# Optimization experiments

Hardware: AMD Instinct MI355X
Metric: run time of the kernel (lower is better)

## Reference

```python
import jax, jax.numpy as jnp
import numpy as np

D_MODEL = 2048
NUM_HEADS = 16
D_K = D_MODEL // NUM_HEADS
LORA_R = 8
LORA_ALPHA = 16
SCALING = LORA_ALPHA / LORA_R  # 2.0
B, S = 2, 2048


def setup_inputs() -> dict:
    key = jax.random.key(0)
    ks = jax.random.split(key, 17)
    s = 1.0 / np.sqrt(D_MODEL)
    d = {"x": jax.random.normal(ks[0], (B, S, D_MODEL), jnp.float32)}
    i = 1
    for name in ("q", "k", "v", "o"):
        d[f"W{name}"] = jax.random.uniform(ks[i], (D_MODEL, D_MODEL), jnp.float32, -s, s); i += 1
        d[f"b{name}"] = jax.random.uniform(ks[i], (D_MODEL,), jnp.float32, -s, s); i += 1
        d[f"A{name}"] = jax.random.uniform(ks[i], (LORA_R, D_MODEL), jnp.float32, -s, s); i += 1
        # lora_B is zero-initialized in the module, but use small random so grads flow meaningfully
        d[f"B{name}"] = jax.random.normal(ks[i], (D_MODEL, LORA_R), jnp.float32) * 0.01; i += 1
    return d


def _lora_linear(x, W, b, A, Bm):
    # F.linear(x, W, b) + (x @ A.T @ B.T) * scaling
    return x @ W.T + b + ((x @ A.T) @ Bm.T) * SCALING


def reference(x, Wq, bq, Aq, Bq, Wk, bk, Ak, Bk, Wv, bv, Av, Bv, Wo, bo, Ao, Bo):
    batch = x.shape[0]
    q = _lora_linear(x, Wq, bq, Aq, Bq)
    k = _lora_linear(x, Wk, bk, Ak, Bk)
    v = _lora_linear(x, Wv, bv, Av, Bv)
    # [B, S, H, Dk] -> [B, H, S, Dk]
    q = q.reshape(batch, -1, NUM_HEADS, D_K).transpose(0, 2, 1, 3)
    k = k.reshape(batch, -1, NUM_HEADS, D_K).transpose(0, 2, 1, 3)
    v = v.reshape(batch, -1, NUM_HEADS, D_K).transpose(0, 2, 1, 3)
    scores = jnp.einsum("bhqd,bhkd->bhqk", q, k) / jnp.sqrt(jnp.float32(D_K))
    attn = jax.nn.softmax(scores, axis=-1)
    context = jnp.einsum("bhqk,bhkd->bhqd", attn, v)
    context = context.transpose(0, 2, 1, 3).reshape(batch, -1, D_MODEL)
    return _lora_linear(context, Wo, bo, Ao, Bo)
```

## Files before the change

### kernel.cpp

```cpp
#include <hip/hip_runtime.h>
#include <stdint.h>

typedef unsigned short u16;
typedef unsigned int   u32;
typedef __bf16  bf16x8 __attribute__((ext_vector_type(8)));
typedef float   f32x4  __attribute__((ext_vector_type(4)));

#define LORA_SCALE 2.0f
#define QSCALE 0.08838834764831845f
#define LOG2E  1.4426950408889634f
#define RESCALE_THR 8.0f

__device__ __forceinline__ u16 f2bf(float f){
  u32 u = __builtin_bit_cast(u32, f);
  u32 r = (u + 0x7fffu + ((u >> 16) & 1u)) >> 16;
  return (u16)r;
}
__device__ __forceinline__ float bf2f(u16 v){
  return __builtin_bit_cast(float, ((u32)v) << 16);
}
__device__ __forceinline__ u32 cvt_pk_bf16(float lo, float hi){
  u32 d;
  asm("v_cvt_pk_bf16_f32 %0, %1, %2" : "=v"(d) : "v"(lo), "v"(hi));
  return d;
}

typedef __attribute__((address_space(3))) u32 lds_u32_t;
typedef __attribute__((address_space(1))) const u32 g_u32_t;

__device__ __forceinline__ void gload16(const void* g, void* l){
  __builtin_amdgcn_global_load_lds((g_u32_t*)(unsigned long long)g,
                                   (lds_u32_t*)(u32)(unsigned long long)l,
                                   16, 0, 0);
}

__global__ __launch_bounds__(256) void cvt_f32_bf16(const float* __restrict__ in,
                                                    u16* __restrict__ out, int n){
  int i = (blockIdx.x * 256 + threadIdx.x) * 8;
  if (i >= n) return;
  float4 a = *(const float4*)(in + i);
  float4 b = *(const float4*)(in + i + 4);
  u16 o[8] = {f2bf(a.x),f2bf(a.y),f2bf(a.z),f2bf(a.w),
              f2bf(b.x),f2bf(b.y),f2bf(b.z),f2bf(b.w)};
  *(uint4*)(out + i) = *(const uint4*)o;
}

template<int NG, int BF16IN>
__global__ __launch_bounds__(256) void lora_xa_kernel(const void* __restrict__ xin,
    const float* __restrict__ A0, const float* __restrict__ A1, const float* __restrict__ A2,
    float* __restrict__ xout){
  int w = threadIdx.x >> 6, lane = threadIdx.x & 63;
  int m = blockIdx.x * 4 + w;
  float acc[NG][8];
  #pragma unroll
  for (int g=0; g<NG; ++g)
    #pragma unroll
    for (int r=0; r<8; ++r) acc[g][r] = 0.f;
  const float* As[3] = {A0, A1, A2};
  #pragma unroll 1
  for (int it=0; it<8; ++it){
    int k = it*256 + lane*4;
    float4 xv;
    if (BF16IN){
      const u16* xp = (const u16*)xin + (size_t)m*2048 + k;
      ushort4 u = *(const ushort4*)xp;
      xv.x = bf2f(u.x); xv.y = bf2f(u.y); xv.z = bf2f(u.z); xv.w = bf2f(u.w);
    } else {
      xv = *(const float4*)((const float*)xin + (size_t)m*2048 + k);
    }
    #pragma unroll
    for (int g=0; g<NG; ++g){
      const float* Ag = As[g];
      #pragma unroll
      for (int r=0; r<8; ++r){
        float4 av = *(const float4*)(Ag + r*2048 + k);
        acc[g][r] += xv.x*av.x + xv.y*av.y + xv.z*av.z + xv.w*av.w;
      }
    }
  }
  #pragma unroll
  for (int g=0; g<NG; ++g)
    #pragma unroll
    for (int r=0; r<8; ++r){
      float v = acc[g][r];
      #pragma unroll
      for (int off=32; off; off>>=1) v += __shfl_xor(v, off);
      if (lane == 0) xout[g*32768 + m*8 + r] = v;
    }
}

__global__ __launch_bounds__(256, 2) void gemm_fused(
    const u16* __restrict__ A, const u16* __restrict__ W,
    const float* __restrict__ bias, const float* __restrict__ lB,
    const float* __restrict__ xa, void* __restrict__ outp,
    int f32out, int swz, float oscale){
  const int Kd = 2048, Nd = 2048;
  __shared__ u16 Ash[128*32];
  __shared__ u16 Bsh[128*32];
  int tid = threadIdx.x, w = tid >> 6, lane = tid & 63;
  int l15 = lane & 15, l4 = lane >> 4;
  int n0 = blockIdx.x * 128, m0 = blockIdx.y * 128;
  int wm = w >> 1, wn = w & 1;
  f32x4 acc[4][4];
  #pragma unroll
  for (int mi=0; mi<4; mi++)
    #pragma unroll
    for (int ni=0; ni<4; ni++) acc[mi][ni] = (f32x4){0.f,0.f,0.f,0.f};

  const u16* Arow = A + (size_t)m0 * Kd;
  const u16* Wrow = W + (size_t)n0 * Kd;
  for (int kt = 0; kt < Kd; kt += 32){
    __syncthreads();
    #pragma unroll
    for (int i=0; i<2; ++i){
      int e = (i*256 + tid) * 8;
      int r = e >> 5, c = e & 31;
      gload16(Arow + (size_t)r*Kd + kt + c, (char*)Ash + i*4096 + w*1024);
      gload16(Wrow + (size_t)r*Kd + kt + c, (char*)Bsh + i*4096 + w*1024);
    }
    __syncthreads();
    bf16x8 af[4], bfv[4];
    #pragma unroll
    for (int mi=0; mi<4; mi++)
      af[mi] = *(const bf16x8*)(Ash + (wm*64 + mi*16 + l15)*32 + l4*8);
    #pragma unroll
    for (int ni=0; ni<4; ni++)
      bfv[ni] = *(const bf16x8*)(Bsh + (wn*64 + ni*16 + l15)*32 + l4*8);
    #pragma unroll
    for (int mi=0; mi<4; mi++)
      #pragma unroll
      for (int ni=0; ni<4; ni++)
        acc[mi][ni] = __builtin_amdgcn_mfma_f32_16x16x32_bf16(af[mi], bfv[ni], acc[mi][ni], 0, 0, 0);
  }
  float bv[4]; float4 lb0[4], lb1[4];
  #pragma unroll
  for (int ni=0; ni<4; ni++){
    int col = n0 + wn*64 + ni*16 + l15;
    bv[ni] = bias[col];
    lb0[ni] = *(const float4*)(lB + col*8);
    lb1[ni] = *(const float4*)(lB + col*8 + 4);
  }
  #pragma unroll
  for (int mi=0; mi<4; mi++)
    #pragma unroll
    for (int j=0; j<4; j++){
      int r = m0 + wm*64 + mi*16 + l4*4 + j;
      float4 xv0 = *(const float4*)(xa + (size_t)r*8);
      float4 xv1 = *(const float4*)(xa + (size_t)r*8 + 4);
      #pragma unroll
      for (int ni=0; ni<4; ni++){
        int col = n0 + wn*64 + ni*16 + l15;
        float v = acc[mi][ni][j] + bv[ni] + LORA_SCALE * (
            xv0.x*lb0[ni].x + xv0.y*lb0[ni].y + xv0.z*lb0[ni].z + xv0.w*lb0[ni].w +
            xv1.x*lb1[ni].x + xv1.y*lb1[ni].y + xv1.z*lb1[ni].z + xv1.w*lb1[ni].w);
        v *= oscale;
        if (f32out){
          ((float*)outp)[(size_t)r*Nd + col] = v;
        } else {
          int cs = swz ? (col ^ ((r & 7) << 3)) : col;
          ((u16*)outp)[(size_t)r*Nd + cs] = f2bf(v);
        }
      }
    }
}

__global__ __launch_bounds__(256) void transpose_v(const u16* __restrict__ V,
                                                   u16* __restrict__ Vt){
  __shared__ u16 tile[64*80];
  int tid = threadIdx.x;
  int f0 = blockIdx.x * 64, m0 = blockIdx.y * 64;
  int i = tid >> 2, j0 = (tid & 3) * 16;
  #pragma unroll
  for (int kk=0; kk<16; kk+=8){
    uint4 u = *(const uint4*)(V + (size_t)(m0 + i)*2048 + f0 + j0 + kk);
    *(uint4*)(tile + i*80 + j0 + kk) = u;
  }
  __syncthreads();
  int j = tid >> 2, i0 = (tid & 3) * 16;
  int b = m0 >> 11, s0 = m0 & 2047;
  int h = f0 >> 7, d = (f0 & 127) + j;
  int c = (d & 7) << 3;
  size_t obase = ((size_t)((b*16 + h)*128 + d)) * 2048 + s0;
  #pragma unroll
  for (int kk=0; kk<16; kk+=8){
    u16 v8[8];
    #pragma unroll
    for (int u2=0; u2<8; ++u2) v8[u2] = tile[(i0+kk+u2)*80 + j];
    *(uint4*)(Vt + obase + ((i0+kk) ^ c)) = *(const uint4*)v8;
  }
}

__global__ __launch_bounds__(256, 2) void attn_kernel(
    const u16* __restrict__ Q, const u16* __restrict__ K,
    const u16* __restrict__ Vt, u16* __restrict__ ctx){
  __shared__ u16 buf[2][16384];
  __shared__ u16 Psh[4*32*64];
  int tid = threadIdx.x, w = tid >> 6, lane = tid & 63;
  int l15 = lane & 15, l4 = lane >> 4;
  int qt = blockIdx.x, bh = blockIdx.y;
  int b = bh >> 4, h = bh & 15;
  const u16* Qg = Q + (size_t)(b*2048 + qt*128) * 2048 + h*128;
  const u16* Kg = K + (size_t)(b*2048) * 2048 + h*128;
  const u16* Vg = Vt + (size_t)bh * 128 * 2048;

  #pragma unroll
  for (int i=0; i<8; ++i){
    int e = (i*256 + tid) * 8;
    int r = e >> 7, cc = e & 127;
    gload16(Qg + (size_t)r*2048 + cc, (char*)buf[1] + i*4096 + w*1024);
  }
  #pragma unroll
  for (int i=0; i<4; ++i){
    int e = (i*256 + tid) * 8;
    int r = e >> 7, cc = e & 127;
    gload16(Kg + (size_t)r*2048 + cc, (char*)buf[0] + i*4096 + w*1024);
    int dd = e >> 6, c2 = e & 63;
    gload16(Vg + (size_t)dd*2048 + c2, (char*)buf[0] + 16384 + i*4096 + w*1024);
  }
  __syncthreads();

  bf16x8 qf[2][4];
  #pragma unroll
  for (int mi=0; mi<2; mi++){
    int r = w*32 + mi*16 + l15;
    #pragma unroll
    for (int kb=0; kb<4; kb++){
      int cc = (kb*32 + l4*8) ^ ((r & 7) << 3);
      qf[mi][kb] = *(const bf16x8*)(buf[1] + r*128 + cc);
    }
  }
  __syncthreads();

  f32x4 ctxa[2][8];
  #pragma unroll
  for (int mi=0; mi<2; mi++)
    #pragma unroll
    for (int nd=0; nd<8; nd++) ctxa[mi][nd] = (f32x4){0.f,0.f,0.f,0.f};
  float mrun[2] = {-3.0e38f, -3.0e38f};
  float lrun[2] = {0.f, 0.f};

  char* PwB = (char*)(Psh + w * (32*64));
  int psw = (l15 & 7) << 4;

  for (int t = 0; t < 32; ++t){
    int cur = t & 1;
    const u16* Kc = buf[cur];
    const u16* Vc = buf[cur] + 8192;
    if (t + 1 < 32){
      int kvn = (t + 1) * 64;
      char* bn = (char*)buf[cur ^ 1];
      #pragma unroll
      for (int i=0; i<4; ++i){
        int e = (i*256 + tid) * 8;
        int r = e >> 7, cc = e & 127;
        gload16(Kg + (size_t)(kvn + r)*2048 + cc, bn + i*4096 + w*1024);
        int dd = e >> 6, c2 = e & 63;
        gload16(Vg + (size_t)dd*2048 + kvn + c2, bn + 16384 + i*4096 + w*1024);
      }
    }
    f32x4 s[2][4];
    #pragma unroll
    for (int mi=0; mi<2; mi++)
      #pragma unroll
      for (int ni=0; ni<4; ni++) s[mi][ni] = (f32x4){0.f,0.f,0.f,0.f};
    __builtin_amdgcn_s_setprio(1);
    #pragma unroll
    for (int kb=0; kb<4; kb++){
      #pragma unroll
      for (int ni=0; ni<4; ni++){
        int r = ni*16 + l15;
        int cc = (kb*32 + l4*8) ^ ((r & 7) << 3);
        bf16x8 kf = *(const bf16x8*)(Kc + r*128 + cc);
        s[0][ni] = __builtin_amdgcn_mfma_f32_16x16x32_bf16(kf, qf[0][kb], s[0][ni], 0, 0, 0);
        s[1][ni] = __builtin_amdgcn_mfma_f32_16x16x32_bf16(kf, qf[1][kb], s[1][ni], 0, 0, 0);
      }
    }
    __builtin_amdgcn_s_setprio(0);
    float pm[2];
    #pragma unroll
    for (int mi=0; mi<2; mi++){
      float v = s[mi][0][0];
      #pragma unroll
      for (int ni=0; ni<4; ni++)
        #pragma unroll
        for (int j=0; j<4; j++) v = fmaxf(v, s[mi][ni][j]);
      v = fmaxf(v, __shfl_xor(v, 16));
      v = fmaxf(v, __shfl_xor(v, 32));
      pm[mi] = v;
    }
    bool need = (pm[0] > mrun[0] + RESCALE_THR) || (pm[1] > mrun[1] + RESCALE_THR);
    if (__any(need)){
      #pragma unroll
      for (int mi=0; mi<2; mi++){
        float mnew = fmaxf(mrun[mi], pm[mi]);
        float cr = exp2f(mrun[mi] - mnew);
        lrun[mi] *= cr;
        mrun[mi] = mnew;
        #pragma unroll
        for (int nd=0; nd<8; nd++) ctxa[mi][nd] *= cr;
      }
    }
    #pragma unroll
    for (int mi=0; mi<2; mi++){
      float ps = 0.f;
      #pragma unroll
      for (int ni=0; ni<4; ni++){
        float p0 = exp2f(s[mi][ni][0] - mrun[mi]);
        float p1 = exp2f(s[mi][ni][1] - mrun[mi]);
        float p2 = exp2f(s[mi][ni][2] - mrun[mi]);
        float p3 = exp2f(s[mi][ni][3] - mrun[mi]);
        ps += (p0 + p1) + (p2 + p3);
        uint2 pk = {cvt_pk_bf16(p0, p1), cvt_pk_bf16(p2, p3)};
        *(uint2*)(PwB + (mi*16 + l15)*128 + ((ni*32 + l4*8) ^ psw)) = pk;
      }
      ps += __shfl_xor(ps, 16);
      ps += __shfl_xor(ps, 32);
      lrun[mi] += ps;
    }
    bf16x8 pb[2][2];
    #pragma unroll
    for (int mi=0; mi<2; mi++)
      #pragma unroll
      for (int kvb=0; kvb<2; kvb++)
        pb[mi][kvb] = *(const bf16x8*)(PwB + (mi*16 + l15)*128 + ((kvb*64 + l4*16) ^ psw));
    __builtin_amdgcn_s_setprio(1);
    #pragma unroll
    for (int nd=0; nd<8; nd++){
      int dd = nd*16 + l15;
      int sw = (dd & 7) << 3;
      #pragma unroll
      for (int kvb=0; kvb<2; kvb++){
        bf16x8 vf = *(const bf16x8*)(Vc + dd*64 + ((kvb*32 + l4*8) ^ sw));
        ctxa[0][nd] = __builtin_amdgcn_mfma_f32_16x16x32_bf16(vf, pb[0][kvb], ctxa[0][nd], 0, 0, 0);
        ctxa[1][nd] = __builtin_amdgcn_mfma_f32_16x16x32_bf16(vf, pb[1][kvb], ctxa[1][nd], 0, 0, 0);
      }
    }
    __builtin_amdgcn_s_setprio(0);
    __syncthreads();
  }
  char* OwB = (char*)buf[0] + w*8192;
  #pragma unroll
  for (int mi=0; mi<2; mi++){
    float inv = 1.0f / lrun[mi];
    #pragma unroll
    for (int nd=0; nd<8; nd++){
      f32x4 c = ctxa[mi][nd] * inv;
      uint2 pk = {cvt_pk_bf16(c[0], c[1]), cvt_pk_bf16(c[2], c[3])};
      *(uint2*)(OwB + (mi*16 + l15)*256 + ((nd*32 + l4*8) ^ psw)) = pk;
    }
  }
  #pragma unroll
  for (int i=0; i<8; ++i){
    int row = i*4 + l4;
    int colb = l15*16;
    uint4 v = *(const uint4*)(OwB + row*256 + (colb ^ ((row & 7) << 4)));
    int srow = qt*128 + w*32 + row;
    *(uint4*)(ctx + ((size_t)(b*2048 + srow))*2048 + h*128 + colb/2) = v;
  }
}

extern "C" void kernel_launch(void* const* d_in, const int* in_sizes, int n_in,
                              void* d_out, int out_size, void* d_ws, size_t ws_size,
                              hipStream_t stream){
  const float* x  = (const float*)d_in[0];
  const float* Wq = (const float*)d_in[1];  const float* bq = (const float*)d_in[2];
  const float* Aq = (const float*)d_in[3];  const float* Bq = (const float*)d_in[4];
  const float* Wk = (const float*)d_in[5];  const float* bk = (const float*)d_in[6];
  const float* Ak = (const float*)d_in[7];  const float* Bk = (const float*)d_in[8];
  const float* Wv = (const float*)d_in[9];  const float* bv = (const float*)d_in[10];
  const float* Av = (const float*)d_in[11]; const float* Bv = (const float*)d_in[12];
  const float* Wo = (const float*)d_in[13]; const float* bo = (const float*)d_in[14];
  const float* Ao = (const float*)d_in[15]; const float* Bo = (const float*)d_in[16];

  char* ws = (char*)d_ws;
  size_t off = 0;
  u16* xbf = (u16*)(ws + off); off += (size_t)4096*2048*2;
  u16* wqb = (u16*)(ws + off); off += (size_t)2048*2048*2;
  u16* wkb = (u16*)(ws + off); off += (size_t)2048*2048*2;
  u16* wvb = (u16*)(ws + off); off += (size_t)2048*2048*2;
  u16* wob = (u16*)(ws + off); off += (size_t)2048*2048*2;
  float* xa = (float*)(ws + off); off += (size_t)4*32768*4;
  u16* Qb  = (u16*)(ws + off); off += (size_t)4096*2048*2;
  u16* Kb  = (u16*)(ws + off); off += (size_t)4096*2048*2;
  u16* Vb  = (u16*)(ws + off); off += (size_t)4096*2048*2;
  u16* Vtb = (u16*)(ws + off); off += (size_t)4096*2048*2;
  if (ws_size < off) return;

  cvt_f32_bf16<<<4096, 256, 0, stream>>>(x,  xbf, 4096*2048);
  cvt_f32_bf16<<<2048, 256, 0, stream>>>(Wq, wqb, 2048*2048);
  cvt_f32_bf16<<<2048, 256, 0, stream>>>(Wk, wkb, 2048*2048);
  cvt_f32_bf16<<<2048, 256, 0, stream>>>(Wv, wvb, 2048*2048);
  cvt_f32_bf16<<<2048, 256, 0, stream>>>(Wo, wob, 2048*2048);

  lora_xa_kernel<3, 0><<<1024, 256, 0, stream>>>((const void*)x, Aq, Ak, Av, xa);

  gemm_fused<<<dim3(16,32), 256, 0, stream>>>(xbf, wqb, bq, Bq, xa,        Qb, 0, 1, QSCALE*LOG2E);
  gemm_fused<<<dim3(16,32), 256, 0, stream>>>(xbf, wkb, bk, Bk, xa+32768,  Kb, 0, 1, 1.0f);
  gemm_fused<<<dim3(16,32), 256, 0, stream>>>(xbf, wvb, bv, Bv, xa+65536,  Vb, 0, 0, 1.0f);

  transpose_v<<<dim3(32,64), 256, 0, stream>>>(Vb, Vtb);

  attn_kernel<<<dim3(16,32), 256, 0, stream>>>(Qb, Kb, Vtb, Vb);

  lora_xa_kernel<1, 1><<<1024, 256, 0, stream>>>((const void*)Vb, Ao, Ao, Ao, xa+98304);

  gemm_fused<<<dim3(16,32), 256, 0, stream>>>(Vb, wob, bo, Bo, xa+98304, d_out, 1, 0, 1.0f);
}
```

Before: 391.7 us.

## Fuse QKV projections into one GEMM launch and merge conversion kernels

The four weight conversions are merged into one launch, and the x-to-bf16 conversion is folded into the LoRA x@A kernel so x is read once. The Q, K and V GEMMs become a single 48x32-block launch over a concatenated bf16 weight buffer, with per-block selection of bias, LoRA B, scale and swizzle. The attention grid is remapped so consecutive blocks spread across heads, which is meant to improve L2 locality or load balance. Together these cut launch overhead and redundant x traffic and give the QKV GEMM more blocks in flight. The cost is extra per-block branching in the fused kernels.

```diff
diff --git a/kernel.cpp b/kernel.cpp
--- a/kernel.cpp
+++ b/kernel.cpp
@@ -34,42 +34,40 @@
                                    16, 0, 0);
 }
 
-__global__ __launch_bounds__(256) void cvt_f32_bf16(const float* __restrict__ in,
-                                                    u16* __restrict__ out, int n){
-  int i = (blockIdx.x * 256 + threadIdx.x) * 8;
-  if (i >= n) return;
-  float4 a = *(const float4*)(in + i);
-  float4 b = *(const float4*)(in + i + 4);
+__global__ __launch_bounds__(256) void cvt_w4(const float* __restrict__ W0,
+    const float* __restrict__ W1, const float* __restrict__ W2,
+    const float* __restrict__ W3, u16* __restrict__ wqkv, u16* __restrict__ wo){
+  int sel = blockIdx.x >> 11;
+  int inner = blockIdx.x & 2047;
+  const float* src = sel==0 ? W0 : sel==1 ? W1 : sel==2 ? W2 : W3;
+  u16* dst = sel<3 ? (wqkv + (size_t)sel*4194304) : wo;
+  int i = (inner*256 + threadIdx.x) * 8;
+  float4 a = *(const float4*)(src + i);
+  float4 b = *(const float4*)(src + i + 4);
   u16 o[8] = {f2bf(a.x),f2bf(a.y),f2bf(a.z),f2bf(a.w),
               f2bf(b.x),f2bf(b.y),f2bf(b.z),f2bf(b.w)};
-  *(uint4*)(out + i) = *(const uint4*)o;
-}
-
-template<int NG, int BF16IN>
-__global__ __launch_bounds__(256) void lora_xa_kernel(const void* __restrict__ xin,
+  *(uint4*)(dst + i) = *(const uint4*)o;
+}
+
+__global__ __launch_bounds__(256) void lora_x_fused(const float* __restrict__ x,
     const float* __restrict__ A0, const float* __restrict__ A1, const float* __restrict__ A2,
-    float* __restrict__ xout){
+    float* __restrict__ xout, u16* __restrict__ xbf){
   int w = threadIdx.x >> 6, lane = threadIdx.x & 63;
   int m = blockIdx.x * 4 + w;
-  float acc[NG][8];
-  #pragma unroll
-  for (int g=0; g<NG; ++g)
+  float acc[3][8];
+  #pragma unroll
+  for (int g=0; g<3; ++g)
     #pragma unroll
     for (int r=0; r<8; ++r) acc[g][r] = 0.f;
   const float* As[3] = {A0, A1, A2};
   #pragma unroll 1
   for (int it=0; it<8; ++it){
     int k = it*256 + lane*4;
-    float4 xv;
-    if (BF16IN){
-      const u16* xp = (const u16*)xin + (size_t)m*2048 + k;
-      ushort4 u = *(const ushort4*)xp;
-      xv.x = bf2f(u.x); xv.y = bf2f(u.y); xv.z = bf2f(u.z); xv.w = bf2f(u.w);
-    } else {
-      xv = *(const float4*)((const float*)xin + (size_t)m*2048 + k);
-    }
-    #pragma unroll
-    for (int g=0; g<NG; ++g){
+    float4 xv = *(const float4*)(x + (size_t)m*2048 + k);
+    u16 o[4] = {f2bf(xv.x), f2bf(xv.y), f2bf(xv.z), f2bf(xv.w)};
+    *(uint2*)(xbf + (size_t)m*2048 + k) = *(const uint2*)o;
+    #pragma unroll
+    for (int g=0; g<3; ++g){
       const float* Ag = As[g];
       #pragma unroll
       for (int r=0; r<8; ++r){
@@ -79,7 +77,7 @@
     }
   }
   #pragma unroll
-  for (int g=0; g<NG; ++g)
+  for (int g=0; g<3; ++g)
     #pragma unroll
     for (int r=0; r<8; ++r){
       float v = acc[g][r];
@@ -89,11 +87,116 @@
     }
 }
 
-__global__ __launch_bounds__(256, 2) void gemm_fused(
+__global__ __launch_bounds__(256) void lora_xa_bf16(const u16* __restrict__ xin,
+    const float* __restrict__ A0, float* __restrict__ xout){
+  int w = threadIdx.x >> 6, lane = threadIdx.x & 63;
+  int m = blockIdx.x * 4 + w;
+  float acc[8];
+  #pragma unroll
+  for (int r=0; r<8; ++r) acc[r] = 0.f;
+  #pragma unroll 1
+  for (int it=0; it<8; ++it){
+    int k = it*256 + lane*4;
+    ushort4 u = *(const ushort4*)(xin + (size_t)m*2048 + k);
+    float4 xv = {bf2f(u.x), bf2f(u.y), bf2f(u.z), bf2f(u.w)};
+    #pragma unroll
+    for (int r=0; r<8; ++r){
+      float4 av = *(const float4*)(A0 + r*2048 + k);
+      acc[r] += xv.x*av.x + xv.y*av.y + xv.z*av.z + xv.w*av.w;
+    }
+  }
+  #pragma unroll
+  for (int r=0; r<8; ++r){
+    float v = acc[r];
+    #pragma unroll
+    for (int off=32; off; off>>=1) v += __shfl_xor(v, off);
+    if (lane == 0) xout[m*8 + r] = v;
+  }
+}
+
+__global__ __launch_bounds__(256, 2) void gemm_qkv(
+    const u16* __restrict__ A, const u16* __restrict__ W,
+    const float* __restrict__ bq, const float* __restrict__ bk, const float* __restrict__ bv,
+    const float* __restrict__ lBq, const float* __restrict__ lBk, const float* __restrict__ lBv,
+    const float* __restrict__ xa, u16* __restrict__ Qb, u16* __restrict__ Kb, u16* __restrict__ Vb){
+  const int Kd = 2048;
+  __shared__ u16 Ash[128*32];
+  __shared__ u16 Bsh[128*32];
+  int tid = threadIdx.x, w = tid >> 6, lane = tid & 63;
+  int l15 = lane & 15, l4 = lane >> 4;
+  int n0g = blockIdx.x * 128, m0 = blockIdx.y * 128;
+  int which = blockIdx.x >> 4;
+  int n0 = n0g & 2047;
+  const float* bias = which==0 ? bq : which==1 ? bk : bv;
+  const float* lB   = which==0 ? lBq : which==1 ? lBk : lBv;
+  const float* xs   = xa + which*32768;
+  u16* outp         = which==0 ? Qb : which==1 ? Kb : Vb;
+  int swz = (which <= 1);
+  float oscale = (which == 0) ? QSCALE*LOG2E : 1.0f;
+  int wm = w >> 1, wn = w & 1;
+  f32x4 acc[4][4];
+  #pragma unroll
+  for (int mi=0; mi<4; mi++)
+    #pragma unroll
+    for (int ni=0; ni<4; ni++) acc[mi][ni] = (f32x4){0.f,0.f,0.f,0.f};
+
+  const u16* Arow = A + (size_t)m0 * Kd;
+  const u16* Wrow = W + (size_t)n0g * Kd;
+  for (int kt = 0; kt < Kd; kt += 32){
+    __syncthreads();
+    #pragma unroll
+    for (int i=0; i<2; ++i){
+      int e = (i*256 + tid) * 8;
+      int r = e >> 5, c = e & 31;
+      gload16(Arow + (size_t)r*Kd + kt + c, (char*)Ash + i*4096 + w*1024);
+      gload16(Wrow + (size_t)r*Kd + kt + c, (char*)Bsh + i*4096 + w*1024);
+    }
+    __syncthreads();
+    bf16x8 af[4], bfv[4];
+    #pragma unroll
+    for (int mi=0; mi<4; mi++)
+      af[mi] = *(const bf16x8*)(Ash + (wm*64 + mi*16 + l15)*32 + l4*8);
+    #pragma unroll
+    for (int ni=0; ni<4; ni++)
+      bfv[ni] = *(const bf16x8*)(Bsh + (wn*64 + ni*16 + l15)*32 + l4*8);
+    #pragma unroll
+    for (int mi=0; mi<4; mi++)
+      #pragma unroll
+      for (int ni=0; ni<4; ni++)
+        acc[mi][ni] = __builtin_amdgcn_mfma_f32_16x16x32_bf16(af[mi], bfv[ni], acc[mi][ni], 0, 0, 0);
+  }
+  float bvv[4]; float4 lb0[4], lb1[4];
+  #pragma unroll
+  for (int ni=0; ni<4; ni++){
+    int col = n0 + wn*64 + ni*16 + l15;
+    bvv[ni] = bias[col];
+    lb0[ni] = *(const float4*)(lB + col*8);
+    lb1[ni] = *(const float4*)(lB + col*8 + 4);
+  }
+  #pragma unroll
+  for (int mi=0; mi<4; mi++)
+    #pragma unroll
+    for (int j=0; j<4; j++){
+      int r = m0 + wm*64 + mi*16 + l4*4 + j;
+      float4 xv0 = *(const float4*)(xs + (size_t)r*8);
+      float4 xv1 = *(const float4*)(xs + (size_t)r*8 + 4);
+      #pragma unroll
+      for (int ni=0; ni<4; ni++){
+        int col = n0 + wn*64 + ni*16 + l15;
+        float v = acc[mi][ni][j] + bvv[ni] + LORA_SCALE * (
+            xv0.x*lb0[ni].x + xv0.y*lb0[ni].y + xv0.z*lb0[ni].z + xv0.w*lb0[ni].w +
+            xv1.x*lb1[ni].x + xv1.y*lb1[ni].y + xv1.z*lb1[ni].z + xv1.w*lb1[ni].w);
+        v *= oscale;
+        int cs = swz ? (col ^ ((r & 7) << 3)) : col;
+        outp[(size_t)r*2048 + cs] = f2bf(v);
+      }
+    }
+}
+
+__global__ __launch_bounds__(256, 2) void gemm_o(
     const u16* __restrict__ A, const u16* __restrict__ W,
     const float* __restrict__ bias, const float* __restrict__ lB,
-    const float* __restrict__ xa, void* __restrict__ outp,
-    int f32out, int swz, float oscale){
+    const float* __restrict__ xa, float* __restrict__ outp){
   const int Kd = 2048, Nd = 2048;
   __shared__ u16 Ash[128*32];
   __shared__ u16 Bsh[128*32];
@@ -153,13 +256,7 @@
         float v = acc[mi][ni][j] + bv[ni] + LORA_SCALE * (
             xv0.x*lb0[ni].x + xv0.y*lb0[ni].y + xv0.z*lb0[ni].z + xv0.w*lb0[ni].w +
             xv1.x*lb1[ni].x + xv1.y*lb1[ni].y + xv1.z*lb1[ni].z + xv1.w*lb1[ni].w);
-        v *= oscale;
-        if (f32out){
-          ((float*)outp)[(size_t)r*Nd + col] = v;
-        } else {
-          int cs = swz ? (col ^ ((r & 7) << 3)) : col;
-          ((u16*)outp)[(size_t)r*Nd + cs] = f2bf(v);
-        }
+        outp[(size_t)r*Nd + col] = v;
       }
     }
 }
@@ -197,7 +294,9 @@
   __shared__ u16 Psh[4*32*64];
   int tid = threadIdx.x, w = tid >> 6, lane = tid & 63;
   int l15 = lane & 15, l4 = lane >> 4;
-  int qt = blockIdx.x, bh = blockIdx.y;
+  int lin = blockIdx.x;
+  int virt = (lin & 7) * 64 + (lin >> 3);
+  int qt = virt & 15, bh = virt >> 4;
   int b = bh >> 4, h = bh & 15;
   const u16* Qg = Q + (size_t)(b*2048 + qt*128) * 2048 + h*128;
   const u16* Kg = K + (size_t)(b*2048) * 2048 + h*128;
@@ -374,11 +473,9 @@
 
   char* ws = (char*)d_ws;
   size_t off = 0;
-  u16* xbf = (u16*)(ws + off); off += (size_t)4096*2048*2;
-  u16* wqb = (u16*)(ws + off); off += (size_t)2048*2048*2;
-  u16* wkb = (u16*)(ws + off); off += (size_t)2048*2048*2;
-  u16* wvb = (u16*)(ws + off); off += (size_t)2048*2048*2;
-  u16* wob = (u16*)(ws + off); off += (size_t)2048*2048*2;
+  u16* xbf  = (u16*)(ws + off); off += (size_t)4096*2048*2;
+  u16* wqkv = (u16*)(ws + off); off += (size_t)3*2048*2048*2;
+  u16* wob  = (u16*)(ws + off); off += (size_t)2048*2048*2;
   float* xa = (float*)(ws + off); off += (size_t)4*32768*4;
   u16* Qb  = (u16*)(ws + off); off += (size_t)4096*2048*2;
   u16* Kb  = (u16*)(ws + off); off += (size_t)4096*2048*2;
@@ -386,23 +483,16 @@
   u16* Vtb = (u16*)(ws + off); off += (size_t)4096*2048*2;
   if (ws_size < off) return;
 
-  cvt_f32_bf16<<<4096, 256, 0, stream>>>(x,  xbf, 4096*2048);
-  cvt_f32_bf16<<<2048, 256, 0, stream>>>(Wq, wqb, 2048*2048);
-  cvt_f32_bf16<<<2048, 256, 0, stream>>>(Wk, wkb, 2048*2048);
-  cvt_f32_bf16<<<2048, 256, 0, stream>>>(Wv, wvb, 2048*2048);
-  cvt_f32_bf16<<<2048, 256, 0, stream>>>(Wo, wob, 2048*2048);
-
-  lora_xa_kernel<3, 0><<<1024, 256, 0, stream>>>((const void*)x, Aq, Ak, Av, xa);
-
-  gemm_fused<<<dim3(16,32), 256, 0, stream>>>(xbf, wqb, bq, Bq, xa,        Qb, 0, 1, QSCALE*LOG2E);
-  gemm_fused<<<dim3(16,32), 256, 0, stream>>>(xbf, wkb, bk, Bk, xa+32768,  Kb, 0, 1, 1.0f);
-  gemm_fused<<<dim3(16,32), 256, 0, stream>>>(xbf, wvb, bv, Bv, xa+65536,  Vb, 0, 0, 1.0f);
+  cvt_w4<<<8192, 256, 0, stream>>>(Wq, Wk, Wv, Wo, wqkv, wob);
+  lora_x_fused<<<1024, 256, 0, stream>>>(x, Aq, Ak, Av, xa, xbf);
+
+  gemm_qkv<<<dim3(48,32), 256, 0, stream>>>(xbf, wqkv, bq, bk, bv, Bq, Bk, Bv, xa, Qb, Kb, Vb);
 
   transpose_v<<<dim3(32,64), 256, 0, stream>>>(Vb, Vtb);
 
-  attn_kernel<<<dim3(16,32), 256, 0, stream>>>(Qb, Kb, Vtb, Vb);
-
-  lora_xa_kernel<1, 1><<<1024, 256, 0, stream>>>((const void*)Vb, Ao, Ao, Ao, xa+98304);
-
-  gemm_fused<<<dim3(16,32), 256, 0, stream>>>(Vb, wob, bo, Bo, xa+98304, d_out, 1, 0, 1.0f);
-}
+  attn_kernel<<<512, 256, 0, stream>>>(Qb, Kb, Vtb, Vb);
+
+  lora_xa_bf16<<<1024, 256, 0, stream>>>(Vb, Ao, xa+98304);
+
+  gemm_o<<<dim3(16,32), 256, 0, stream>>>(Vb, wob, bo, Bo, xa+98304, (float*)d_out);
+}
```

After: 364.9 us. -6.8%, faster.
